# Kernel optimization log

Measured on AMD Instinct MI355X. Metric: run time of the kernel, lower is better.

## Reference

```python
import jax, jax.numpy as jnp
import numpy as np

E = 8          # num_ensemble
S = 512        # state_dim
A = 64         # action_dim
H = 2048       # hidden_dim
L = 3          # num_layers - 1 residual hidden blocks
B = 8192
LN_EPS = 1e-5


def _xavier(key, shape, gain=1.0):
    fan_in, fan_out = shape[-2], shape[-1]
    a = gain * np.sqrt(6.0 / (fan_in + fan_out))
    return jax.random.uniform(key, shape, jnp.float32, -a, a)


def setup_inputs() -> dict:
    key = jax.random.key(0)
    ks = jax.random.split(key, 12)
    inp = {
        "state": jax.random.normal(ks[0], (B, S), jnp.float32),
        "action": jax.random.normal(ks[1], (B, A), jnp.float32),
        # input projection
        "W_in": _xavier(ks[2], (E, S + A, H)),
        "b_in": jnp.zeros((E, H), jnp.float32),
        "g_in": jnp.ones((E, H), jnp.float32),
        "be_in": jnp.zeros((E, H), jnp.float32),
        # hidden residual blocks
        "W_h": _xavier(ks[3], (E, L, H, H)),
        "b_h": jnp.zeros((E, L, H), jnp.float32),
        "g_h": jnp.ones((E, L, H), jnp.float32),
        "be_h": jnp.zeros((E, L, H), jnp.float32),
        # output heads
        "W_state": _xavier(ks[4], (E, H, S), gain=0.1),
        "b_state": jnp.zeros((E, S), jnp.float32),
        "W_rew": _xavier(ks[5], (E, H, 1)),
        "b_rew": jnp.zeros((E, 1), jnp.float32),
        "W_done": _xavier(ks[6], (E, H, 1)),
        "b_done": jnp.zeros((E, 1), jnp.float32),
    }
    return inp


def _layernorm(x, g, b):
    # x: [E, B, H]; g, b: [E, 1, H]
    mu = jnp.mean(x, axis=-1, keepdims=True)
    var = jnp.mean(jnp.square(x - mu), axis=-1, keepdims=True)
    return (x - mu) * jax.lax.rsqrt(var + LN_EPS) * g + b


def reference(state, action, W_in, b_in, g_in, be_in, W_h, b_h, g_h, be_h,
              W_state, b_state, W_rew, b_rew, W_done, b_done):
    x = jnp.concatenate([state, action], axis=-1)  # [B, S+A]
    # input proj for all heads: [E, B, H]
    h = jnp.einsum('bi,eih->ebh', x, W_in) + b_in[:, None, :]
    h = jax.nn.gelu(_layernorm(h, g_in[:, None, :], be_in[:, None, :]), approximate=False)
    for l in range(L):
        z = jnp.einsum('ebh,ehk->ebk', h, W_h[:, l]) + b_h[:, l, None, :]
        z = jax.nn.gelu(_layernorm(z, g_h[:, l, None, :], be_h[:, l, None, :]), approximate=False)
        h = z + h
    next_states = state[None] + jnp.einsum('ebh,ehs->ebs', h, W_state) + b_state[:, None, :]
    rewards = jnp.einsum('ebh,eho->ebo', h, W_rew) + b_rew[:, None, :]
    dones = jax.nn.sigmoid(jnp.einsum('ebh,eho->ebo', h, W_done) + b_done[:, None, :])
    mean_state = jnp.mean(next_states, axis=0)          # [B, S]
    mean_reward = jnp.mean(rewards, axis=0)             # [B, 1]
    mean_done = jnp.mean(dones, axis=0)                 # [B, 1]
    # torch.var default is unbiased (correction=1)
    var_state = jnp.var(next_states, axis=0, ddof=1)
    uncertainty = jnp.mean(var_state, axis=-1)          # [B]
    return (mean_state, mean_reward, mean_done, uncertainty)
```

## Files before the change

### kernel.cpp

```cpp
#include <hip/hip_runtime.h>
#include <stdint.h>

#define B_SZ  8192
#define S_DIM 512
#define H_DIM 2048
#define KIN   576
#define OUT_MS 4194304

typedef unsigned short u16;
typedef u16   u16x8 __attribute__((ext_vector_type(8)));
typedef u16   u16x4 __attribute__((ext_vector_type(4)));
typedef short s16x8 __attribute__((ext_vector_type(8)));
typedef float f32x4 __attribute__((ext_vector_type(4)));

__device__ __forceinline__ float b2f(u16 u) {
    union { unsigned int i; float f; } v; v.i = ((unsigned int)u) << 16; return v.f;
}
__device__ __forceinline__ u16 f2b(float f) {
    union { float f; unsigned int i; } v; v.f = f;
    unsigned int u = v.i;
    return (u16)((u + 0x7FFFu + ((u >> 16) & 1u)) >> 16);
}
__device__ __forceinline__ float gelu_f(float y) {
    const float t = __expf(-1.5957691216f * y * (1.0f + 0.044715f * y * y));
    return y / (1.0f + t);
}

__device__ __forceinline__ void gload_lds16(const void* gp, void* lp) {
    __builtin_amdgcn_global_load_lds(
        (const __attribute__((address_space(1))) unsigned int*)gp,
        (__attribute__((address_space(3))) unsigned int*)(unsigned int)(uintptr_t)lp,
        16, 0, 0);
}

#define MFMA __builtin_amdgcn_mfma_f32_16x16x32_bf16

__global__ __launch_bounds__(256) void k_concat(
    const float* __restrict__ state, const float* __restrict__ action,
    u16* __restrict__ xb)
{
    int idx = blockIdx.x * 256 + threadIdx.x;
    int b = idx / KIN, c = idx - b * KIN;
    float v = (c < S_DIM) ? state[(size_t)b * S_DIM + c]
                          : action[(size_t)b * 64 + (c - S_DIM)];
    xb[idx] = f2b(v);
}

__global__ __launch_bounds__(256) void k_cast(
    const float* __restrict__ p0, const float* __restrict__ p1,
    const float* __restrict__ p2, const float* __restrict__ p3,
    const float* __restrict__ p4, const float* __restrict__ p5,
    u16* __restrict__ dst)
{
    int i = blockIdx.x * 256 + threadIdx.x;
    float v;
    if      (i < 16384)  v = p0[i];
    else if (i < 32768)  v = p1[i - 16384];
    else if (i < 81920)  v = p2[i - 32768];
    else if (i < 131072) v = p3[i - 81920];
    else if (i < 147456) v = p4[i - 131072];
    else                 v = p5[i - 147456];
    dst[i] = f2b(v);
}

__global__ __launch_bounds__(256) void k_transpose(
    const float* __restrict__ src, u16* __restrict__ dst, int R, int C)
{
    __shared__ float tile[32][33];
    const int tx = threadIdx.x, ty = threadIdx.y;
    const int c0 = blockIdx.x * 32, r0 = blockIdx.y * 32;
    const size_t mo = (size_t)blockIdx.z * R * C;
    src += mo; dst += mo;
#pragma unroll
    for (int j = 0; j < 4; ++j)
        tile[ty + j * 8][tx] = src[(size_t)(r0 + ty + j * 8) * C + c0 + tx];
    __syncthreads();
#pragma unroll
    for (int j = 0; j < 4; ++j)
        dst[(size_t)(c0 + ty + j * 8) * R + r0 + tx] = f2b(tile[tx][ty + j * 8]);
}

template<int MODE>
__global__ __launch_bounds__(512, 2) void k_gemm256(
    const u16* __restrict__ A, size_t sAe,
    const u16* __restrict__ Bt, size_t sBe,
    const float* __restrict__ bias, int sbE,
    void* __restrict__ Zv, size_t sZe,
    const float* __restrict__ st, float* __restrict__ sum_o, float* __restrict__ sq_o,
    int N, int K)
{
    __shared__ __align__(16) u16 lds[5][16384];
    const int t = threadIdx.x;
    const int lane = t & 63;
    const int wid = t >> 6;
    const int wm = wid >> 2, wn = wid & 3;

    const int gx = gridDim.x, gy = gridDim.y;
    const int linb = blockIdx.x + gx * (blockIdx.y + gy * blockIdx.z);
    const int x  = linb & 7;
    const int s  = linb >> 3;
    const int m_ = (gx * gy) >> 3;
    const int bz = s / m_;
    const int r_ = s - bz * m_;
    const int p_ = r_ / gy;
    const int by = r_ - p_ * gy;
    const int bx = x * (gx >> 3) + p_;
    const int m0 = bx * 256, n0 = by * 256;

    const u16* Ab = A + (size_t)bz * sAe + (size_t)m0 * K;
    const u16* Bb = Bt + (size_t)bz * sBe + (size_t)n0 * K;

    const int srow = t >> 3;
    const int scol = (((t & 7) ^ (srow & 7)) * 8);
    const int ldst = srow * 64 + (t & 7) * 8;
    const int NT = K >> 6;

    const u16* gA = Ab + (size_t)srow * K + scol;
    const u16* gB = Bb + (size_t)srow * K + scol;
    auto STG = [&](int kt, int mat, int r, u16* slab) {
        const u16* gp = (mat ? gB : gA) + (size_t)(r * 64) * K + kt * 64;
        gload_lds16(gp, slab + r * 4096 + ldst);
    };

    const int fr = lane & 15, hi = lane >> 4;
    const int cswz = (fr & 7) << 4;
    const int ac0 = (hi * 16) ^ cswz;
    const int ac1 = (64 + hi * 16) ^ cswz;
    const int ar0 = (wm * 128 + fr) * 128;
    const int ar1 = (wm * 128 + 16 + fr) * 128;
    int boff[4][2];
#pragma unroll
    for (int nj = 0; nj < 4; ++nj) {
        const int br_ = (wn * 64 + nj * 16 + fr) * 128;
        boff[nj][0] = br_ + ac0;
        boff[nj][1] = br_ + ac1;
    }

    f32x4 acc[8][4];
#pragma unroll
    for (int i = 0; i < 8; ++i)
#pragma unroll
        for (int j = 0; j < 4; ++j) acc[i][j] = (f32x4){0.f, 0.f, 0.f, 0.f};

    s16x8 bfrag[4][2];
    s16x8 af[4];

    u16* pa0 = &lds[0][0];
    u16* pa1 = &lds[1][0];
    u16* pa2 = &lds[2][0];
    u16* pb0 = &lds[3][0];
    u16* pb1 = &lds[4][0];

#define LOADB(PB)                                                         \
    _Pragma("unroll") for (int nj = 0; nj < 4; ++nj) {                    \
        bfrag[nj][0] = *(const s16x8*)((const char*)(PB) + boff[nj][0]);  \
        bfrag[nj][1] = *(const s16x8*)((const char*)(PB) + boff[nj][1]);  \
    }
#define LOADA(PA, Q)                                                      \
    af[0] = *(const s16x8*)((const char*)(PA) + (Q) * 4096 + ar0 + ac0);  \
    af[1] = *(const s16x8*)((const char*)(PA) + (Q) * 4096 + ar0 + ac1);  \
    af[2] = *(const s16x8*)((const char*)(PA) + (Q) * 4096 + ar1 + ac0);  \
    af[3] = *(const s16x8*)((const char*)(PA) + (Q) * 4096 + ar1 + ac1);
#define DOMFMA(Q)                                                         \
    __builtin_amdgcn_s_barrier();                                         \
    asm volatile("s_waitcnt lgkmcnt(0)" ::: "memory");                    \
    __builtin_amdgcn_sched_barrier(0);                                    \
    __builtin_amdgcn_s_setprio(1);                                        \
    _Pragma("unroll") for (int nj = 0; nj < 4; ++nj) {                    \
        acc[2*(Q)][nj]   = MFMA(bfrag[nj][0], af[0], acc[2*(Q)][nj], 0, 0, 0);   \
        acc[2*(Q)][nj]   = MFMA(bfrag[nj][1], af[1], acc[2*(Q)][nj], 0, 0, 0);   \
        acc[2*(Q)+1][nj] = MFMA(bfrag[nj][0], af[2], acc[2*(Q)+1][nj], 0, 0, 0); \
        acc[2*(Q)+1][nj] = MFMA(bfrag[nj][1], af[3], acc[2*(Q)+1][nj], 0, 0, 0); \
    }                                                                     \
    __builtin_amdgcn_s_setprio(0);

    STG(0, 0, 0, pa0); STG(0, 0, 1, pa0); STG(0, 0, 2, pa0); STG(0, 0, 3, pa0);
    STG(0, 1, 0, pb0); STG(0, 1, 1, pb0); STG(0, 1, 2, pb0); STG(0, 1, 3, pb0);
    if (NT > 1) {
        STG(1, 0, 0, pa1); STG(1, 0, 1, pa1); STG(1, 0, 2, pa1); STG(1, 0, 3, pa1);
        asm volatile("s_waitcnt vmcnt(4)" ::: "memory");
    } else {
        asm volatile("s_waitcnt vmcnt(0)" ::: "memory");
    }
    __builtin_amdgcn_sched_barrier(0);
    __builtin_amdgcn_s_barrier();

    for (int kt = 0; kt < NT; ++kt) {
        const bool h1 = kt + 1 < NT, h2 = kt + 2 < NT;
        LOADB(pb0) LOADA(pa0, 0)
        if (h1) { STG(kt + 1, 1, 0, pb1); STG(kt + 1, 1, 1, pb1);
                  STG(kt + 1, 1, 2, pb1); STG(kt + 1, 1, 3, pb1); }
        DOMFMA(0)
        __builtin_amdgcn_s_barrier();
        LOADA(pa0, 1)
        if (h2) { STG(kt + 2, 0, 0, pa2); STG(kt + 2, 0, 2, pa2); }
        DOMFMA(1)
        __builtin_amdgcn_s_barrier();
        LOADA(pa0, 2)
        if (h2) { STG(kt + 2, 0, 1, pa2); STG(kt + 2, 0, 3, pa2); }
        DOMFMA(2)
        __builtin_amdgcn_s_barrier();
        LOADA(pa0, 3)
        DOMFMA(3)
        if (h2) { asm volatile("s_waitcnt vmcnt(4)" ::: "memory"); }
        else    { asm volatile("s_waitcnt vmcnt(0)" ::: "memory"); }
        __builtin_amdgcn_sched_barrier(0);
        __builtin_amdgcn_s_barrier();
        u16* ta = pa0; pa0 = pa1; pa1 = pa2; pa2 = ta;
        u16* tb = pb0; pb0 = pb1; pb1 = tb;
    }
#undef LOADB
#undef LOADA
#undef DOMFMA

    const float* biasp = bias + (size_t)bz * sbE;
    f32x4 bias4[4];
#pragma unroll
    for (int nj = 0; nj < 4; ++nj)
        bias4[nj] = *(const f32x4*)&biasp[n0 + wn * 64 + nj * 16 + hi * 4];
#pragma unroll
    for (int mi = 0; mi < 8; ++mi) {
        const int row = m0 + wm * 128 + mi * 16 + fr;
#pragma unroll
        for (int nj = 0; nj < 4; ++nj) {
            const int cb = n0 + wn * 64 + nj * 16 + hi * 4;
            const size_t idx = (size_t)row * N + cb;
            if (MODE == 0) {
                u16x4 o;
#pragma unroll
                for (int r = 0; r < 4; ++r) o[r] = f2b(acc[mi][nj][r] + bias4[nj][r]);
                *(u16x4*)&((u16*)Zv)[(size_t)bz * sZe + idx] = o;
            } else if (MODE == 1) {
                const f32x4 sv = *(const f32x4*)&st[idx];
                f32x4 c;
#pragma unroll
                for (int r = 0; r < 4; ++r) c[r] = sv[r] + acc[mi][nj][r] + bias4[nj][r];
                *(f32x4*)&((float*)Zv)[(size_t)bz * sZe + idx] = c;
            } else {
                const f32x4 sv = *(const f32x4*)&st[idx];
                f32x4 s1 = *(const f32x4*)&sum_o[idx];
                f32x4 s2 = *(const f32x4*)&sq_o[idx];
#pragma unroll
                for (int r = 0; r < 4; ++r) {
                    const float c = sv[r] + acc[mi][nj][r] + bias4[nj][r];
                    s1[r] += c; s2[r] += c * c;
                }
                *(f32x4*)&sum_o[idx] = s1;
                *(f32x4*)&sq_o[idx] = s2;
            }
        }
    }
}

template<int RES, int FIN>
__global__ __launch_bounds__(256) void k_ln(
    const u16* __restrict__ z, u16* __restrict__ h,
    const u16* __restrict__ g, const u16* __restrict__ be, int egb,
    const u16* __restrict__ wr, const u16* __restrict__ wd,
    const float* __restrict__ br, const float* __restrict__ bd,
    float* __restrict__ sum_rew, float* __restrict__ sum_done)
{
    const int lane = threadIdx.x & 63;
    const int w = threadIdx.x >> 6;
    const int e = blockIdx.z;
    const int row0 = blockIdx.x * 8 + w * 2;
    const size_t base0 = ((size_t)e * B_SZ + row0) * H_DIM;
    const u16* gp = g + (size_t)e * egb;
    const u16* bp = be + (size_t)e * egb;

    u16x8 zv[2][4], gv[4], bv[4], hv[2][4];
#pragma unroll
    for (int j = 0; j < 4; ++j) {
        const int c = j * 512 + lane * 8;
        zv[0][j] = *(const u16x8*)&z[base0 + c];
        zv[1][j] = *(const u16x8*)&z[base0 + H_DIM + c];
        gv[j] = *(const u16x8*)&gp[c];
        bv[j] = *(const u16x8*)&bp[c];
        if (RES) {
            hv[0][j] = *(const u16x8*)&h[base0 + c];
            hv[1][j] = *(const u16x8*)&h[base0 + H_DIM + c];
        }
    }
    float s0 = 0.f, q0 = 0.f, s1 = 0.f, q1 = 0.f;
#pragma unroll
    for (int j = 0; j < 4; ++j)
#pragma unroll
        for (int k = 0; k < 8; ++k) {
            const float f0 = b2f(zv[0][j][k]); s0 += f0; q0 += f0 * f0;
            const float f1 = b2f(zv[1][j][k]); s1 += f1; q1 += f1 * f1;
        }
#pragma unroll
    for (int o = 32; o; o >>= 1) {
        s0 += __shfl_xor(s0, o); q0 += __shfl_xor(q0, o);
        s1 += __shfl_xor(s1, o); q1 += __shfl_xor(q1, o);
    }
    const float mu0 = s0 * (1.0f / H_DIM);
    const float rs0 = rsqrtf(q0 * (1.0f / H_DIM) - mu0 * mu0 + 1e-5f);
    const float mu1 = s1 * (1.0f / H_DIM);
    const float rs1 = rsqrtf(q1 * (1.0f / H_DIM) - mu1 * mu1 + 1e-5f);

    float dr0 = 0.f, dd0 = 0.f, dr1 = 0.f, dd1 = 0.f;
#pragma unroll
    for (int j = 0; j < 4; ++j) {
        const int c = j * 512 + lane * 8;
        u16x8 wrv, wdv;
        if (FIN) {
            wrv = *(const u16x8*)&wr[(size_t)e * H_DIM + c];
            wdv = *(const u16x8*)&wd[(size_t)e * H_DIM + c];
        }
        u16x8 ov0, ov1;
#pragma unroll
        for (int k = 0; k < 8; ++k) {
            const float gk = b2f(gv[j][k]), bk = b2f(bv[j][k]);
            const float y0 = (b2f(zv[0][j][k]) - mu0) * rs0 * gk + bk;
            const float y1 = (b2f(zv[1][j][k]) - mu1) * rs1 * gk + bk;
            float g0 = gelu_f(y0), g1 = gelu_f(y1);
            if (RES) { g0 += b2f(hv[0][j][k]); g1 += b2f(hv[1][j][k]); }
            if (FIN) {
                const float wrk = b2f(wrv[k]), wdk = b2f(wdv[k]);
                dr0 += g0 * wrk; dd0 += g0 * wdk;
                dr1 += g1 * wrk; dd1 += g1 * wdk;
            }
            ov0[k] = f2b(g0); ov1[k] = f2b(g1);
        }
        *(u16x8*)&h[base0 + c] = ov0;
        *(u16x8*)&h[base0 + H_DIM + c] = ov1;
    }
    if (FIN) {
#pragma unroll
        for (int o = 32; o; o >>= 1) {
            dr0 += __shfl_xor(dr0, o); dd0 += __shfl_xor(dd0, o);
            dr1 += __shfl_xor(dr1, o); dd1 += __shfl_xor(dd1, o);
        }
        if (lane == 0) {
            atomicAdd(&sum_rew[row0], dr0 + br[e]);
            atomicAdd(&sum_done[row0], 1.0f / (1.0f + __expf(-(dd0 + bd[e]))));
            atomicAdd(&sum_rew[row0 + 1], dr1 + br[e]);
            atomicAdd(&sum_done[row0 + 1], 1.0f / (1.0f + __expf(-(dd1 + bd[e]))));
        }
    }
}

__global__ __launch_bounds__(256) void k_rewdone(
    const u16* __restrict__ hB, const float* __restrict__ Wr, const float* __restrict__ Wd,
    const float* __restrict__ br, const float* __restrict__ bd,
    float* __restrict__ sum_rew, float* __restrict__ sum_done)
{
    const int e = blockIdx.z;
    const int lane = threadIdx.x & 63;
    const int b = blockIdx.x * 4 + (threadIdx.x >> 6);
    const u16* hrow = hB + ((size_t)e * B_SZ + b) * H_DIM;
    const float* wr_ = Wr + (size_t)e * H_DIM;
    const float* wd_ = Wd + (size_t)e * H_DIM;
    float dr = 0.f, dd = 0.f;
#pragma unroll
    for (int j = 0; j < 4; ++j) {
        const int o = j * 512 + lane * 8;
        u16x8 hv = *(const u16x8*)&hrow[o];
#pragma unroll
        for (int k = 0; k < 8; ++k) {
            const float f = b2f(hv[k]);
            dr += f * wr_[o + k];
            dd += f * wd_[o + k];
        }
    }
#pragma unroll
    for (int o = 32; o; o >>= 1) { dr += __shfl_xor(dr, o); dd += __shfl_xor(dd, o); }
    if (lane == 0) {
        atomicAdd(&sum_rew[b], dr + br[e]);
        atomicAdd(&sum_done[b], 1.0f / (1.0f + expf(-(dd + bd[e]))));
    }
}

template<int FB>
__global__ __launch_bounds__(256) void k_final(
    const float* __restrict__ P, const float* __restrict__ sum_st,
    const float* __restrict__ sq_st, const float* __restrict__ sum_rew,
    const float* __restrict__ sum_done, float* __restrict__ out)
{
    const int b = blockIdx.x, t = threadIdx.x;
    float vs = 0.f;
#pragma unroll
    for (int k = 0; k < 2; ++k) {
        const int s = t + k * 256;
        const size_t i = (size_t)b * S_DIM + s;
        float S1, S2;
        if (FB == 0) {
            S1 = 0.f; S2 = 0.f;
#pragma unroll
            for (int e = 0; e < 8; ++e) {
                const float c = P[(size_t)e * OUT_MS + i];
                S1 += c; S2 += c * c;
            }
        } else { S1 = sum_st[i]; S2 = sq_st[i]; }
        out[i] = S1 * 0.125f;
        vs += (S2 - S1 * S1 * 0.125f) * (1.0f / 7.0f);
    }
#pragma unroll
    for (int o = 32; o; o >>= 1) vs += __shfl_xor(vs, o);
    __shared__ float rv[4];
    if ((t & 63) == 0) rv[t >> 6] = vs;
    __syncthreads();
    if (t == 0) {
        const float tot = rv[0] + rv[1] + rv[2] + rv[3];
        out[OUT_MS + b] = sum_rew[b] * 0.125f;
        out[OUT_MS + B_SZ + b] = sum_done[b] * 0.125f;
        out[OUT_MS + 2 * B_SZ + b] = tot * (1.0f / S_DIM);
    }
}

extern "C" void kernel_launch(void* const* d_in, const int* in_sizes, int n_in,
                              void* d_out, int out_size, void* d_ws, size_t ws_size,
                              hipStream_t stream) {
    (void)in_sizes; (void)n_in; (void)out_size;
    const float* state   = (const float*)d_in[0];
    const float* action  = (const float*)d_in[1];
    const float* W_in    = (const float*)d_in[2];
    const float* b_in    = (const float*)d_in[3];
    const float* g_in    = (const float*)d_in[4];
    const float* be_in   = (const float*)d_in[5];
    const float* W_h     = (const float*)d_in[6];
    const float* b_h     = (const float*)d_in[7];
    const float* g_h     = (const float*)d_in[8];
    const float* be_h    = (const float*)d_in[9];
    const float* W_state = (const float*)d_in[10];
    const float* b_state = (const float*)d_in[11];
    const float* W_rew   = (const float*)d_in[12];
    const float* b_rew   = (const float*)d_in[13];
    const float* W_done  = (const float*)d_in[14];
    const float* b_done  = (const float*)d_in[15];
    float* out = (float*)d_out;

    char* ws = (char*)d_ws;
    size_t off = 0;
    auto alloc = [&](size_t bytes) -> void* {
        void* p = ws + off; off += (bytes + 255) & ~((size_t)255); return p;
    };
    const size_t BH = (size_t)B_SZ * H_DIM;
    u16*   xb      = (u16*)alloc((size_t)B_SZ * KIN * 2);
    u16*   Wt_in   = (u16*)alloc((size_t)8 * H_DIM * KIN * 2);
    u16*   Wt_h    = (u16*)alloc((size_t)24 * H_DIM * H_DIM * 2);
    u16*   Wt_st   = (u16*)alloc((size_t)8 * S_DIM * H_DIM * 2);
    u16*   gb16    = (u16*)alloc((size_t)163840 * 2);
    float* sum_st  = (float*)alloc((size_t)B_SZ * S_DIM * 4);
    float* sq_st   = (float*)alloc((size_t)B_SZ * S_DIM * 4);
    float* sum_rew = (float*)alloc((size_t)B_SZ * 4);
    float* sum_done= (float*)alloc((size_t)B_SZ * 4);
    const size_t fixed = off;
    const int EB = (ws_size >= fixed + 2ULL * 8 * BH * 2) ? 8 : 1;
    u16*   hbuf    = (u16*)alloc((size_t)EB * BH * 2);
    u16*   zbuf    = (u16*)alloc((size_t)EB * BH * 2);
    float* Pbuf    = (float*)zbuf;

    u16* g16_in = gb16;
    u16* be16_in = gb16 + 16384;
    u16* g16_h = gb16 + 32768;
    u16* be16_h = gb16 + 81920;
    u16* wr16 = gb16 + 131072;
    u16* wd16 = gb16 + 147456;

    if (EB == 8) {
        hipMemsetAsync(sum_rew, 0, 2 * (size_t)B_SZ * 4, stream);
    } else {
        hipMemsetAsync(sum_st, 0, (2 * (size_t)B_SZ * S_DIM + 2 * B_SZ) * 4, stream);
    }

    k_concat<<<dim3((B_SZ * KIN) / 256), dim3(256), 0, stream>>>(state, action, xb);
    k_cast<<<dim3(640), dim3(256), 0, stream>>>(g_in, be_in, g_h, be_h, W_rew, W_done, gb16);
    k_transpose<<<dim3(H_DIM / 32, KIN / 32, 8),    dim3(32, 8), 0, stream>>>(W_in, Wt_in, KIN, H_DIM);
    k_transpose<<<dim3(H_DIM / 32, H_DIM / 32, 24), dim3(32, 8), 0, stream>>>(W_h, Wt_h, H_DIM, H_DIM);
    k_transpose<<<dim3(S_DIM / 32, H_DIM / 32, 8),  dim3(32, 8), 0, stream>>>(W_state, Wt_st, H_DIM, S_DIM);

    for (int e0 = 0; e0 < 8; e0 += EB) {
        const dim3 gH(32, 8, EB), gS(32, 2, EB), gL(B_SZ / 8, 1, EB), gF(B_SZ / 4, 1, EB);
        k_gemm256<0><<<gH, 512, 0, stream>>>(
            xb, 0, Wt_in + (size_t)e0 * H_DIM * KIN, (size_t)H_DIM * KIN,
            b_in + (size_t)e0 * H_DIM, H_DIM, zbuf, BH,
            nullptr, nullptr, nullptr, H_DIM, KIN);
        k_ln<0, 0><<<gL, 256, 0, stream>>>(zbuf, hbuf,
            g16_in + (size_t)e0 * H_DIM, be16_in + (size_t)e0 * H_DIM, H_DIM,
            nullptr, nullptr, nullptr, nullptr, nullptr, nullptr);
        for (int l = 0; l < 3; ++l) {
            k_gemm256<0><<<gH, 512, 0, stream>>>(
                hbuf, BH, Wt_h + ((size_t)e0 * 3 + l) * H_DIM * H_DIM, (size_t)3 * H_DIM * H_DIM,
                b_h + (size_t)(e0 * 3 + l) * H_DIM, 3 * H_DIM, zbuf, BH,
                nullptr, nullptr, nullptr, H_DIM, H_DIM);
            if (EB == 8 && l == 2) {
                k_ln<1, 1><<<gL, 256, 0, stream>>>(zbuf, hbuf,
                    g16_h + (size_t)(e0 * 3 + l) * H_DIM, be16_h + (size_t)(e0 * 3 + l) * H_DIM,
                    3 * H_DIM, wr16, wd16, b_rew, b_done, sum_rew, sum_done);
            } else {
                k_ln<1, 0><<<gL, 256, 0, stream>>>(zbuf, hbuf,
                    g16_h + (size_t)(e0 * 3 + l) * H_DIM, be16_h + (size_t)(e0 * 3 + l) * H_DIM,
                    3 * H_DIM, nullptr, nullptr, nullptr, nullptr, nullptr, nullptr);
            }
        }
        if (EB == 8) {
            k_gemm256<1><<<gS, 512, 0, stream>>>(
                hbuf, BH, Wt_st, (size_t)S_DIM * H_DIM,
                b_state, S_DIM, (void*)Pbuf, (size_t)OUT_MS,
                state, nullptr, nullptr, S_DIM, H_DIM);
        } else {
            k_gemm256<2><<<gS, 512, 0, stream>>>(
                hbuf, BH, Wt_st + (size_t)e0 * S_DIM * H_DIM, (size_t)S_DIM * H_DIM,
                b_state + (size_t)e0 * S_DIM, S_DIM, (void*)zbuf, 0,
                state, sum_st, sq_st, S_DIM, H_DIM);
            k_rewdone<<<gF, 256, 0, stream>>>(hbuf,
                W_rew + (size_t)e0 * H_DIM, W_done + (size_t)e0 * H_DIM,
                b_rew + e0, b_done + e0, sum_rew, sum_done);
        }
    }
    if (EB == 8)
        k_final<0><<<dim3(B_SZ), dim3(256), 0, stream>>>(Pbuf, nullptr, nullptr, sum_rew, sum_done, out);
    else
        k_final<1><<<dim3(B_SZ), dim3(256), 0, stream>>>(nullptr, sum_st, sq_st, sum_rew, sum_done, out);
}
```

Before: 2.655 ms.

## Pre-pack weights into MFMA fragment order and load B directly to registers

Replaces the weight transpose with a kernel that packs weights into per-wave MFMA fragment layout. The GEMM then loads B fragments straight from global memory into registers instead of staging them through LDS. The A pipeline drops from triple to double buffering with fewer barriers per k-tile. This cuts LDS traffic and footprint, but each wave now fetches its own B from global or L2 with less prefetch depth, which risks exposing memory latency.

New measurement: 2.994 ms. +12.8%, slower.

```diff
diff --git a/kernel.cpp b/kernel.cpp
--- a/kernel.cpp
+++ b/kernel.cpp
@@ -63,33 +63,34 @@
     dst[i] = f2b(v);
 }
 
-__global__ __launch_bounds__(256) void k_transpose(
-    const float* __restrict__ src, u16* __restrict__ dst, int R, int C)
-{
-    __shared__ float tile[32][33];
-    const int tx = threadIdx.x, ty = threadIdx.y;
-    const int c0 = blockIdx.x * 32, r0 = blockIdx.y * 32;
-    const size_t mo = (size_t)blockIdx.z * R * C;
-    src += mo; dst += mo;
-#pragma unroll
-    for (int j = 0; j < 4; ++j)
-        tile[ty + j * 8][tx] = src[(size_t)(r0 + ty + j * 8) * C + c0 + tx];
-    __syncthreads();
-#pragma unroll
-    for (int j = 0; j < 4; ++j)
-        dst[(size_t)(c0 + ty + j * 8) * R + r0 + tx] = f2b(tile[tx][ty + j * 8]);
+__global__ __launch_bounds__(256) void k_wfrag16(
+    const float* __restrict__ W, u16* __restrict__ Wf, int Kd, int Nd)
+{
+    const int NKT = Kd >> 6;
+    const int gid = blockIdx.x * 256 + threadIdx.x;
+    const int lane = gid & 63, lid = gid >> 6;
+    const int h = lid & 1, rest = lid >> 1;
+    const int kt = rest % NKT, fnb = rest / NKT;
+    const int n = fnb * 16 + (lane & 15);
+    const int k0 = kt * 64 + h * 32 + (lane >> 4) * 8;
+    const size_t mo = (size_t)blockIdx.z * Kd * Nd;
+    const float* src = W + mo + (size_t)k0 * Nd + n;
+    u16x8 o;
+#pragma unroll
+    for (int j = 0; j < 8; ++j) o[j] = f2b(src[(size_t)j * Nd]);
+    *(u16x8*)&Wf[mo + (size_t)lid * 512 + lane * 8] = o;
 }
 
 template<int MODE>
 __global__ __launch_bounds__(512, 2) void k_gemm256(
     const u16* __restrict__ A, size_t sAe,
-    const u16* __restrict__ Bt, size_t sBe,
+    const u16* __restrict__ Wf, size_t sBe,
     const float* __restrict__ bias, int sbE,
     void* __restrict__ Zv, size_t sZe,
     const float* __restrict__ st, float* __restrict__ sum_o, float* __restrict__ sq_o,
     int N, int K)
 {
-    __shared__ __align__(16) u16 lds[5][16384];
+    __shared__ __align__(16) u16 lds[2][16384];
     const int t = threadIdx.x;
     const int lane = t & 63;
     const int wid = t >> 6;
@@ -108,19 +109,20 @@
     const int m0 = bx * 256, n0 = by * 256;
 
     const u16* Ab = A + (size_t)bz * sAe + (size_t)m0 * K;
-    const u16* Bb = Bt + (size_t)bz * sBe + (size_t)n0 * K;
-
     const int srow = t >> 3;
     const int scol = (((t & 7) ^ (srow & 7)) * 8);
     const int ldst = srow * 64 + (t & 7) * 8;
     const int NT = K >> 6;
-
     const u16* gA = Ab + (size_t)srow * K + scol;
-    const u16* gB = Bb + (size_t)srow * K + scol;
-    auto STG = [&](int kt, int mat, int r, u16* slab) {
-        const u16* gp = (mat ? gB : gA) + (size_t)(r * 64) * K + kt * 64;
-        gload_lds16(gp, slab + r * 4096 + ldst);
+    auto STGA = [&](int kt, u16* slab) {
+#pragma unroll
+        for (int r = 0; r < 4; ++r)
+            gload_lds16(gA + (size_t)(r * 64) * K + kt * 64, slab + r * 4096 + ldst);
     };
+
+    const int NKT = NT;
+    const u16* wq = Wf + (size_t)bz * sBe
+                  + (size_t)((n0 >> 4) + wn * 4) * NKT * 1024 + (size_t)lane * 8;
 
     const int fr = lane & 15, hi = lane >> 4;
     const int cswz = (fr & 7) << 4;
@@ -128,13 +130,6 @@
     const int ac1 = (64 + hi * 16) ^ cswz;
     const int ar0 = (wm * 128 + fr) * 128;
     const int ar1 = (wm * 128 + 16 + fr) * 128;
-    int boff[4][2];
-#pragma unroll
-    for (int nj = 0; nj < 4; ++nj) {
-        const int br_ = (wn * 64 + nj * 16 + fr) * 128;
-        boff[nj][0] = br_ + ac0;
-        boff[nj][1] = br_ + ac1;
-    }
 
     f32x4 acc[8][4];
 #pragma unroll
@@ -142,76 +137,59 @@
 #pragma unroll
         for (int j = 0; j < 4; ++j) acc[i][j] = (f32x4){0.f, 0.f, 0.f, 0.f};
 
-    s16x8 bfrag[4][2];
+    s16x8 bf0[4][2], bf1[4][2];
     s16x8 af[4];
-
-    u16* pa0 = &lds[0][0];
-    u16* pa1 = &lds[1][0];
-    u16* pa2 = &lds[2][0];
-    u16* pb0 = &lds[3][0];
-    u16* pb1 = &lds[4][0];
-
-#define LOADB(PB)                                                         \
+    u16* slab0 = &lds[0][0];
+    u16* slab1 = &lds[1][0];
+
+#define LOADBG(BF, KT)                                                    \
     _Pragma("unroll") for (int nj = 0; nj < 4; ++nj) {                    \
-        bfrag[nj][0] = *(const s16x8*)((const char*)(PB) + boff[nj][0]);  \
-        bfrag[nj][1] = *(const s16x8*)((const char*)(PB) + boff[nj][1]);  \
+        const u16* p_ = wq + ((size_t)nj * NKT + (KT)) * 1024;            \
+        BF[nj][0] = *(const s16x8*)(p_);                                  \
+        BF[nj][1] = *(const s16x8*)(p_ + 512);                            \
     }
 #define LOADA(PA, Q)                                                      \
     af[0] = *(const s16x8*)((const char*)(PA) + (Q) * 4096 + ar0 + ac0);  \
     af[1] = *(const s16x8*)((const char*)(PA) + (Q) * 4096 + ar0 + ac1);  \
     af[2] = *(const s16x8*)((const char*)(PA) + (Q) * 4096 + ar1 + ac0);  \
     af[3] = *(const s16x8*)((const char*)(PA) + (Q) * 4096 + ar1 + ac1);
-#define DOMFMA(Q)                                                         \
-    __builtin_amdgcn_s_barrier();                                         \
-    asm volatile("s_waitcnt lgkmcnt(0)" ::: "memory");                    \
-    __builtin_amdgcn_sched_barrier(0);                                    \
+#define QMFMA(Q, BFC)                                                     \
     __builtin_amdgcn_s_setprio(1);                                        \
     _Pragma("unroll") for (int nj = 0; nj < 4; ++nj) {                    \
-        acc[2*(Q)][nj]   = MFMA(bfrag[nj][0], af[0], acc[2*(Q)][nj], 0, 0, 0);   \
-        acc[2*(Q)][nj]   = MFMA(bfrag[nj][1], af[1], acc[2*(Q)][nj], 0, 0, 0);   \
-        acc[2*(Q)+1][nj] = MFMA(bfrag[nj][0], af[2], acc[2*(Q)+1][nj], 0, 0, 0); \
-        acc[2*(Q)+1][nj] = MFMA(bfrag[nj][1], af[3], acc[2*(Q)+1][nj], 0, 0, 0); \
+        acc[2*(Q)][nj]   = MFMA(BFC[nj][0], af[0], acc[2*(Q)][nj], 0, 0, 0);   \
+        acc[2*(Q)][nj]   = MFMA(BFC[nj][1], af[1], acc[2*(Q)][nj], 0, 0, 0);   \
+        acc[2*(Q)+1][nj] = MFMA(BFC[nj][0], af[2], acc[2*(Q)+1][nj], 0, 0, 0); \
+        acc[2*(Q)+1][nj] = MFMA(BFC[nj][1], af[3], acc[2*(Q)+1][nj], 0, 0, 0); \
     }                                                                     \
     __builtin_amdgcn_s_setprio(0);
-
-    STG(0, 0, 0, pa0); STG(0, 0, 1, pa0); STG(0, 0, 2, pa0); STG(0, 0, 3, pa0);
-    STG(0, 1, 0, pb0); STG(0, 1, 1, pb0); STG(0, 1, 2, pb0); STG(0, 1, 3, pb0);
-    if (NT > 1) {
-        STG(1, 0, 0, pa1); STG(1, 0, 1, pa1); STG(1, 0, 2, pa1); STG(1, 0, 3, pa1);
-        asm volatile("s_waitcnt vmcnt(4)" ::: "memory");
-    } else {
-        asm volatile("s_waitcnt vmcnt(0)" ::: "memory");
-    }
+#define TILE(KT, BFC, BFN, LAc, LAn) {                                    \
+    const bool h1_ = (KT) + 1 < NT;                                       \
+    if (h1_) { STGA((KT) + 1, LAn); LOADBG(BFN, (KT) + 1) }               \
+    LOADA(LAc, 0) QMFMA(0, BFC)                                           \
+    LOADA(LAc, 1) QMFMA(1, BFC)                                           \
+    LOADA(LAc, 2) QMFMA(2, BFC)                                           \
+    LOADA(LAc, 3) QMFMA(3, BFC)                                           \
+    if (h1_) { asm volatile("s_waitcnt vmcnt(8)" ::: "memory"); }         \
+    else     { asm volatile("s_waitcnt vmcnt(0)" ::: "memory"); }         \
+    __builtin_amdgcn_sched_barrier(0);                                    \
+    __builtin_amdgcn_s_barrier(); }
+
+    STGA(0, slab0);
+    LOADBG(bf0, 0)
+    asm volatile("s_waitcnt vmcnt(8)" ::: "memory");
     __builtin_amdgcn_sched_barrier(0);
     __builtin_amdgcn_s_barrier();
 
-    for (int kt = 0; kt < NT; ++kt) {
-        const bool h1 = kt + 1 < NT, h2 = kt + 2 < NT;
-        LOADB(pb0) LOADA(pa0, 0)
-        if (h1) { STG(kt + 1, 1, 0, pb1); STG(kt + 1, 1, 1, pb1);
-                  STG(kt + 1, 1, 2, pb1); STG(kt + 1, 1, 3, pb1); }
-        DOMFMA(0)
-        __builtin_amdgcn_s_barrier();
-        LOADA(pa0, 1)
-        if (h2) { STG(kt + 2, 0, 0, pa2); STG(kt + 2, 0, 2, pa2); }
-        DOMFMA(1)
-        __builtin_amdgcn_s_barrier();
-        LOADA(pa0, 2)
-        if (h2) { STG(kt + 2, 0, 1, pa2); STG(kt + 2, 0, 3, pa2); }
-        DOMFMA(2)
-        __builtin_amdgcn_s_barrier();
-        LOADA(pa0, 3)
-        DOMFMA(3)
-        if (h2) { asm volatile("s_waitcnt vmcnt(4)" ::: "memory"); }
-        else    { asm volatile("s_waitcnt vmcnt(0)" ::: "memory"); }
-        __builtin_amdgcn_sched_barrier(0);
-        __builtin_amdgcn_s_barrier();
-        u16* ta = pa0; pa0 = pa1; pa1 = pa2; pa2 = ta;
-        u16* tb = pb0; pb0 = pb1; pb1 = tb;
-    }
-#undef LOADB
+    int kt = 0;
+    for (; kt + 1 < NT; kt += 2) {
+        TILE(kt, bf0, bf1, slab0, slab1)
+        TILE(kt + 1, bf1, bf0, slab1, slab0)
+    }
+    if (kt < NT) { TILE(kt, bf0, bf1, slab0, slab1) }
+#undef LOADBG
 #undef LOADA
-#undef DOMFMA
+#undef QMFMA
+#undef TILE
 
     const float* biasp = bias + (size_t)bz * sbE;
     f32x4 bias4[4];
@@ -438,9 +416,9 @@
     };
     const size_t BH = (size_t)B_SZ * H_DIM;
     u16*   xb      = (u16*)alloc((size_t)B_SZ * KIN * 2);
-    u16*   Wt_in   = (u16*)alloc((size_t)8 * H_DIM * KIN * 2);
-    u16*   Wt_h    = (u16*)alloc((size_t)24 * H_DIM * H_DIM * 2);
-    u16*   Wt_st   = (u16*)alloc((size_t)8 * S_DIM * H_DIM * 2);
+    u16*   Wf_in   = (u16*)alloc((size_t)8 * H_DIM * KIN * 2);
+    u16*   Wf_h    = (u16*)alloc((size_t)24 * H_DIM * H_DIM * 2);
+    u16*   Wf_st   = (u16*)alloc((size_t)8 * S_DIM * H_DIM * 2);
     u16*   gb16    = (u16*)alloc((size_t)163840 * 2);
     float* sum_st  = (float*)alloc((size_t)B_SZ * S_DIM * 4);
     float* sq_st   = (float*)alloc((size_t)B_SZ * S_DIM * 4);
@@ -467,14 +445,14 @@
 
     k_concat<<<dim3((B_SZ * KIN) / 256), dim3(256), 0, stream>>>(state, action, xb);
     k_cast<<<dim3(640), dim3(256), 0, stream>>>(g_in, be_in, g_h, be_h, W_rew, W_done, gb16);
-    k_transpose<<<dim3(H_DIM / 32, KIN / 32, 8),    dim3(32, 8), 0, stream>>>(W_in, Wt_in, KIN, H_DIM);
-    k_transpose<<<dim3(H_DIM / 32, H_DIM / 32, 24), dim3(32, 8), 0, stream>>>(W_h, Wt_h, H_DIM, H_DIM);
-    k_transpose<<<dim3(S_DIM / 32, H_DIM / 32, 8),  dim3(32, 8), 0, stream>>>(W_state, Wt_st, H_DIM, S_DIM);
+    k_wfrag16<<<dim3(576, 1, 8),   dim3(256), 0, stream>>>(W_in, Wf_in, KIN, H_DIM);
+    k_wfrag16<<<dim3(2048, 1, 24), dim3(256), 0, stream>>>(W_h, Wf_h, H_DIM, H_DIM);
+    k_wfrag16<<<dim3(512, 1, 8),   dim3(256), 0, stream>>>(W_state, Wf_st, H_DIM, S_DIM);
 
     for (int e0 = 0; e0 < 8; e0 += EB) {
         const dim3 gH(32, 8, EB), gS(32, 2, EB), gL(B_SZ / 8, 1, EB), gF(B_SZ / 4, 1, EB);
         k_gemm256<0><<<gH, 512, 0, stream>>>(
-            xb, 0, Wt_in + (size_t)e0 * H_DIM * KIN, (size_t)H_DIM * KIN,
+            xb, 0, Wf_in + (size_t)e0 * H_DIM * KIN, (size_t)H_DIM * KIN,
             b_in + (size_t)e0 * H_DIM, H_DIM, zbuf, BH,
             nullptr, nullptr, nullptr, H_DIM, KIN);
         k_ln<0, 0><<<gL, 256, 0, stream>>>(zbuf, hbuf,
@@ -482,7 +460,7 @@
             nullptr, nullptr, nullptr, nullptr, nullptr, nullptr);
         for (int l = 0; l < 3; ++l) {
             k_gemm256<0><<<gH, 512, 0, stream>>>(
-                hbuf, BH, Wt_h + ((size_t)e0 * 3 + l) * H_DIM * H_DIM, (size_t)3 * H_DIM * H_DIM,
+                hbuf, BH, Wf_h + ((size_t)e0 * 3 + l) * H_DIM * H_DIM, (size_t)3 * H_DIM * H_DIM,
                 b_h + (size_t)(e0 * 3 + l) * H_DIM, 3 * H_DIM, zbuf, BH,
                 nullptr, nullptr, nullptr, H_DIM, H_DIM);
             if (EB == 8 && l == 2) {
@@ -497,12 +475,12 @@
         }
         if (EB == 8) {
             k_gemm256<1><<<gS, 512, 0, stream>>>(
-                hbuf, BH, Wt_st, (size_t)S_DIM * H_DIM,
+                hbuf, BH, Wf_st, (size_t)S_DIM * H_DIM,
                 b_state, S_DIM, (void*)Pbuf, (size_t)OUT_MS,
                 state, nullptr, nullptr, S_DIM, H_DIM);
         } else {
             k_gemm256<2><<<gS, 512, 0, stream>>>(
-                hbuf, BH, Wt_st + (size_t)e0 * S_DIM * H_DIM, (size_t)S_DIM * H_DIM,
+                hbuf, BH, Wf_st + (size_t)e0 * S_DIM * H_DIM, (size_t)S_DIM * H_DIM,
                 b_state + (size_t)e0 * S_DIM, S_DIM, (void*)zbuf, 0,
                 state, sum_st, sq_st, S_DIM, H_DIM);
             k_rewdone<<<gF, 256, 0, stream>>>(hbuf,
```
